# Kernel optimization log

Hardware: AMD Instinct MI355X
Metric: run time of the kernel (lower is better)

Reference implementation:

```python
import jax, jax.numpy as jnp
import numpy as np

ATT = 256  # att_fc_size
MIN_W = 32  # min_width_feat
EPS = 1e-5  # InstanceNorm eps


def setup_inputs() -> dict:
    key = jax.random.key(0)
    ks = jax.random.split(key, 16)
    B, C, H, W = 32, 256, 128, 256
    hid = 256
    s = 0.02
    inp = {
        'features': jax.random.normal(ks[0], (B, C, H, W), jnp.float32),
        'prev_attn_weights': jax.random.uniform(ks[1], (B, H), jnp.float32),
        'coverage_vector': jax.random.uniform(ks[2], (B, H), jnp.float32) * 2.0,
        'hidden_h': jax.random.normal(ks[3], (1, B, hid), jnp.float32),
        # dense_width: Linear(min_width, 1)
        'w_width': jax.random.normal(ks[4], (MIN_W, 1), jnp.float32) * s,
        'b_width': jnp.zeros((1,), jnp.float32),
        # dense_enc: Linear(C, att)
        'w_enc': jax.random.normal(ks[5], (C, ATT), jnp.float32) * s,
        'b_enc': jnp.zeros((ATT,), jnp.float32),
        # conv_block: Conv1d(2, 16, k=15, pad=7)  (OIW layout)
        'conv_w': jax.random.normal(ks[6], (16, 2, 15), jnp.float32) * s,
        'conv_b': jnp.zeros((16,), jnp.float32),
        # dense_conv_block: Linear(16, att)
        'w_cb': jax.random.normal(ks[7], (16, ATT), jnp.float32) * s,
        'b_cb': jnp.zeros((ATT,), jnp.float32),
        # dense_hidden: Linear(hidden, att)
        'w_hid': jax.random.normal(ks[8], (hid, ATT), jnp.float32) * s,
        'b_hid': jnp.zeros((ATT,), jnp.float32),
        # dense_align: Linear(att, 1)
        'w_align': jax.random.normal(ks[9], (ATT, 1), jnp.float32) * s,
        'b_align': jnp.zeros((1,), jnp.float32),
    }
    return inp


def reference(features, prev_attn_weights, coverage_vector, hidden_h,
              w_width, b_width, w_enc, b_enc, conv_w, conv_b,
              w_cb, b_cb, w_hid, b_hid, w_align, b_align):
    B, C, H, W = features.shape
    # AdaptiveMaxPool2d((None, MIN_W)) with W % MIN_W == 0 -> uniform window max
    hf = features.reshape(B, C, H, MIN_W, W // MIN_W).max(axis=-1)  # (B,C,H,MIN_W)
    # dense_width -> (B,C,H)
    h_features = (jnp.einsum('bchm,mo->bcho', hf, w_width) + b_width)[..., 0]
    # branch 1: dense_enc on (B,H,C)
    s = jnp.einsum('bhc,ca->bha', h_features.transpose(0, 2, 1), w_enc) + b_enc
    # location + coverage channels: (B,2,H)
    cat = jnp.stack([prev_attn_weights, jnp.clip(coverage_vector, 0.0, 1.0)], axis=1)
    # InstanceNorm1d (no affine): per (b, channel) over H
    mu = cat.mean(axis=-1, keepdims=True)
    var = cat.var(axis=-1, keepdims=True)
    cat = (cat - mu) * jax.lax.rsqrt(var + EPS)
    # Conv1d(2 -> 16, k=15, pad=7)
    conv = jax.lax.conv_general_dilated(
        cat, conv_w, window_strides=(1,), padding=[(7, 7)],
        dimension_numbers=('NCH', 'OIH', 'NCH')) + conv_b[None, :, None]  # (B,16,H)
    s = s + jnp.einsum('bhk,ka->bha', conv.transpose(0, 2, 1), w_cb) + b_cb
    # hidden branch: (1,B,hid) -> (1,B,att) -> (B,1,att), broadcasts over H
    hsum = (jnp.einsum('lbd,da->lba', hidden_h, w_hid) + b_hid).transpose(1, 0, 2)
    s = s + hsum
    s = jnp.tanh(s)
    align_score = jnp.einsum('bha,ao->bho', s, w_align) + b_align  # (B,H,1)
    attn = jax.nn.softmax(align_score, axis=1)  # softmax over H
    # context: features^T(H<->W) @ attn -> (B,C,W)
    context = jnp.einsum('bchw,bh->bcw', features, attn[..., 0])
    return context, attn[..., 0]
```

## Files before the change

### kernel.cpp

```cpp
#include <hip/hip_runtime.h>
#include <hip/hip_bf16.h>

#define B_DIM 32
#define C_DIM 256
#define H_DIM 128
#define W_DIM 256
#define ATT_DIM 256

__global__ __launch_bounds__(256) void k1_pool_width(
    const float* __restrict__ feat, const float* __restrict__ w_width,
    const float* __restrict__ b_width, float* __restrict__ hfT)
{
  const int lane = threadIdx.x & 63;
  const long r = (long)blockIdx.x * 4 + (threadIdx.x >> 6);
  const float* p = feat + (size_t)r * W_DIM + lane * 4;
  float4 v4 = *reinterpret_cast<const float4*>(p);
  float v = fmaxf(fmaxf(v4.x, v4.y), fmaxf(v4.z, v4.w));
  v = fmaxf(v, __shfl_xor(v, 1));
  float contrib = (lane & 1) ? 0.0f : v * w_width[lane >> 1];
#pragma unroll
  for (int off = 32; off >= 1; off >>= 1) contrib += __shfl_xor(contrib, off);
  if (lane == 0) {
    int b = (int)(r >> 15);
    int c = ((int)r >> 7) & 255;
    int h = (int)r & 127;
    hfT[((size_t)(b * H_DIM + h)) * C_DIM + c] = contrib + b_width[0];
  }
}

__global__ __launch_bounds__(128) void k2_norm_conv(
    const float* __restrict__ prev, const float* __restrict__ cov,
    const float* __restrict__ conv_w, const float* __restrict__ conv_b,
    float* __restrict__ convT)
{
  const int b = blockIdx.x, h = threadIdx.x;
  const int lane = h & 63, wid = h >> 6;
  __shared__ float n0[H_DIM], n1[H_DIM];
  __shared__ float ws4[2][4];
  __shared__ float cw[16 * 2 * 15];
  for (int i = h; i < 480; i += 128) cw[i] = conv_w[i];
  float x0 = prev[b * H_DIM + h];
  float x1 = cov[b * H_DIM + h];
  x1 = fminf(fmaxf(x1, 0.0f), 1.0f);
  float s0 = x0, q0 = x0 * x0, s1 = x1, q1 = x1 * x1;
#pragma unroll
  for (int off = 32; off >= 1; off >>= 1) {
    s0 += __shfl_xor(s0, off); q0 += __shfl_xor(q0, off);
    s1 += __shfl_xor(s1, off); q1 += __shfl_xor(q1, off);
  }
  if (lane == 0) { ws4[wid][0] = s0; ws4[wid][1] = q0; ws4[wid][2] = s1; ws4[wid][3] = q1; }
  __syncthreads();
  float S0 = ws4[0][0] + ws4[1][0], Q0 = ws4[0][1] + ws4[1][1];
  float S1 = ws4[0][2] + ws4[1][2], Q1 = ws4[0][3] + ws4[1][3];
  const float rH = 1.0f / H_DIM;
  float mu0 = S0 * rH, mu1 = S1 * rH;
  float var0 = Q0 * rH - mu0 * mu0;
  float var1 = Q1 * rH - mu1 * mu1;
  float inv0 = 1.0f / sqrtf(var0 + 1e-5f);
  float inv1 = 1.0f / sqrtf(var1 + 1e-5f);
  n0[h] = (x0 - mu0) * inv0;
  n1[h] = (x1 - mu1) * inv1;
  __syncthreads();
  float o[16];
#pragma unroll
  for (int k = 0; k < 16; k++) o[k] = conv_b[k];
#pragma unroll
  for (int j = 0; j < 15; j++) {
    int hh = h - 7 + j;
    if (hh >= 0 && hh < H_DIM) {
      float f0 = n0[hh], f1 = n1[hh];
#pragma unroll
      for (int k = 0; k < 16; k++)
        o[k] += f0 * cw[k * 30 + j] + f1 * cw[k * 30 + 15 + j];
    }
  }
  float* outp = convT + ((size_t)(b * H_DIM + h)) * 16;
#pragma unroll
  for (int k = 0; k < 16; k++) outp[k] = o[k];
}

__global__ __launch_bounds__(256) void k2b_hsum(
    const float* __restrict__ hidden, const float* __restrict__ w_hid,
    const float* __restrict__ b_hid, const float* __restrict__ b_enc,
    const float* __restrict__ b_cb, float* __restrict__ hsum)
{
  const int b = blockIdx.x, a = threadIdx.x;
  float acc = b_hid[a] + b_enc[a] + b_cb[a];
  const float* hb = hidden + b * 256;
#pragma unroll 4
  for (int d = 0; d < 256; d++) acc += hb[d] * w_hid[d * ATT_DIM + a];
  hsum[b * ATT_DIM + a] = acc;
}

__global__ __launch_bounds__(256) void k3_gemm_align(
    const float* __restrict__ hfT, const float* __restrict__ convT,
    const float* __restrict__ hsum, const float* __restrict__ w_enc,
    const float* __restrict__ w_cb, const float* __restrict__ w_align,
    const float* __restrict__ b_align, float* __restrict__ align_out)
{
  __shared__ float At[C_DIM][20];
  __shared__ float Ct[16][17];
  __shared__ float red[16][ATT_DIM];
  const int tid = threadIdx.x;
  const int m0 = blockIdx.x * 16;
  const int b = m0 >> 7;
#pragma unroll
  for (int i = 0; i < 16; i++)
    At[tid][i] = hfT[(size_t)(m0 + i) * C_DIM + tid];
  {
    int m = tid >> 4, k = tid & 15;
    Ct[k][m] = convT[(size_t)m0 * 16 + tid];
  }
  __syncthreads();
  float acc[16];
#pragma unroll
  for (int m = 0; m < 16; m++) acc[m] = 0.0f;
  const float* wep = w_enc + tid;
#pragma unroll 4
  for (int k = 0; k < C_DIM; k++) {
    float bv = wep[k * ATT_DIM];
    const float4 a0 = *reinterpret_cast<const float4*>(&At[k][0]);
    const float4 a1 = *reinterpret_cast<const float4*>(&At[k][4]);
    const float4 a2 = *reinterpret_cast<const float4*>(&At[k][8]);
    const float4 a3 = *reinterpret_cast<const float4*>(&At[k][12]);
    acc[0] += a0.x * bv; acc[1] += a0.y * bv; acc[2] += a0.z * bv; acc[3] += a0.w * bv;
    acc[4] += a1.x * bv; acc[5] += a1.y * bv; acc[6] += a1.z * bv; acc[7] += a1.w * bv;
    acc[8] += a2.x * bv; acc[9] += a2.y * bv; acc[10] += a2.z * bv; acc[11] += a2.w * bv;
    acc[12] += a3.x * bv; acc[13] += a3.y * bv; acc[14] += a3.z * bv; acc[15] += a3.w * bv;
  }
#pragma unroll
  for (int k = 0; k < 16; k++) {
    float bv = w_cb[k * ATT_DIM + tid];
#pragma unroll
    for (int m = 0; m < 16; m++) acc[m] += Ct[k][m] * bv;
  }
  const float hs = hsum[b * ATT_DIM + tid];
  const float wa = w_align[tid];
#pragma unroll
  for (int m = 0; m < 16; m++)
    red[m][tid] = tanhf(acc[m] + hs) * wa;
  __syncthreads();
  const int lane = tid & 63, wid = tid >> 6;
  const float ba = b_align[0];
  for (int m = wid; m < 16; m += 4) {
    float s = red[m][lane] + red[m][lane + 64] + red[m][lane + 128] + red[m][lane + 192];
#pragma unroll
    for (int off = 32; off >= 1; off >>= 1) s += __shfl_xor(s, off);
    if (lane == 0) align_out[m0 + m] = s + ba;
  }
}

__global__ __launch_bounds__(128) void k4_softmax(
    const float* __restrict__ align, float* __restrict__ attn)
{
  const int b = blockIdx.x, h = threadIdx.x;
  const int lane = h & 63, wid = h >> 6;
  __shared__ float sm[2], ss[2];
  float x = align[b * H_DIM + h];
  float m = x;
#pragma unroll
  for (int off = 32; off >= 1; off >>= 1) m = fmaxf(m, __shfl_xor(m, off));
  if (lane == 0) sm[wid] = m;
  __syncthreads();
  m = fmaxf(sm[0], sm[1]);
  float e = expf(x - m);
  float s = e;
#pragma unroll
  for (int off = 32; off >= 1; off >>= 1) s += __shfl_xor(s, off);
  if (lane == 0) ss[wid] = s;
  __syncthreads();
  s = ss[0] + ss[1];
  attn[b * H_DIM + h] = e / s;
}

__global__ __launch_bounds__(256) void k5_context(
    const float* __restrict__ feat, const float* __restrict__ attn,
    float* __restrict__ ctx)
{
  const int bc = blockIdx.x;
  const int b = bc >> 8;
  const int tid = threadIdx.x;
  __shared__ float at[H_DIM];
  if (tid < H_DIM) at[tid] = attn[(b << 7) + tid];
  __syncthreads();
  const int g = tid >> 6, lane = tid & 63;
  const float* base = feat + (size_t)bc * H_DIM * W_DIM;
  float4 acc = make_float4(0.f, 0.f, 0.f, 0.f);
  for (int h = g; h < H_DIM; h += 4) {
    float4 v = *reinterpret_cast<const float4*>(base + h * W_DIM + lane * 4);
    float a = at[h];
    acc.x += v.x * a; acc.y += v.y * a; acc.z += v.z * a; acc.w += v.w * a;
  }
  __shared__ float4 part[4][64];
  part[g][lane] = acc;
  __syncthreads();
  if (tid < 64) {
    float4 r0 = part[0][tid], r1 = part[1][tid], r2 = part[2][tid], r3 = part[3][tid];
    float4 o;
    o.x = r0.x + r1.x + r2.x + r3.x;
    o.y = r0.y + r1.y + r2.y + r3.y;
    o.z = r0.z + r1.z + r2.z + r3.z;
    o.w = r0.w + r1.w + r2.w + r3.w;
    *reinterpret_cast<float4*>(ctx + (size_t)bc * W_DIM + tid * 4) = o;
  }
}

extern "C" void kernel_launch(void* const* d_in, const int* in_sizes, int n_in,
                              void* d_out, int out_size, void* d_ws, size_t ws_size,
                              hipStream_t stream)
{
  const float* feat    = (const float*)d_in[0];
  const float* prev    = (const float*)d_in[1];
  const float* cov     = (const float*)d_in[2];
  const float* hidden  = (const float*)d_in[3];
  const float* w_width = (const float*)d_in[4];
  const float* b_width = (const float*)d_in[5];
  const float* w_enc   = (const float*)d_in[6];
  const float* b_enc   = (const float*)d_in[7];
  const float* conv_w  = (const float*)d_in[8];
  const float* conv_b  = (const float*)d_in[9];
  const float* w_cb    = (const float*)d_in[10];
  const float* b_cb    = (const float*)d_in[11];
  const float* w_hid   = (const float*)d_in[12];
  const float* b_hid   = (const float*)d_in[13];
  const float* w_align = (const float*)d_in[14];
  const float* b_align = (const float*)d_in[15];

  float* ctx_out  = (float*)d_out;
  float* attn_out = (float*)d_out + (size_t)B_DIM * C_DIM * W_DIM;

  float* ws    = (float*)d_ws;
  float* hfT   = ws;
  float* convT = hfT + 1048576;
  float* hsum  = convT + 65536;
  float* align = hsum + 8192;

  k1_pool_width<<<dim3((B_DIM * C_DIM * H_DIM) / 4), dim3(256), 0, stream>>>(
      feat, w_width, b_width, hfT);
  k2_norm_conv<<<dim3(B_DIM), dim3(128), 0, stream>>>(prev, cov, conv_w, conv_b, convT);
  k2b_hsum<<<dim3(B_DIM), dim3(256), 0, stream>>>(hidden, w_hid, b_hid, b_enc, b_cb, hsum);
  k3_gemm_align<<<dim3((B_DIM * H_DIM) / 16), dim3(256), 0, stream>>>(
      hfT, convT, hsum, w_enc, w_cb, w_align, b_align, align);
  k4_softmax<<<dim3(B_DIM), dim3(128), 0, stream>>>(align, attn_out);
  k5_context<<<dim3(B_DIM * C_DIM), dim3(256), 0, stream>>>(feat, attn_out, ctx_out);
}
```

Baseline: 493.5 us.

## Fuse small kernels, reverse context block order for L2 reuse, shrink GEMM tile

Merges the pooling, norm+conv and hidden-projection kernels into one launch. The pooling part now gives each block one (b,c) slab and writes hf in B,C,H layout with coalesced stores. The softmax moves into the context kernel, which runs its blocks in reverse order so recently pooled feature slabs may still sit in L2. The align GEMM tile shrinks from 16 to 8 rows to launch more blocks. This cuts launch count and the scattered transposed stores, at the cost of recomputing the softmax in every context block.

Result: faster. 400.6 us (-18.8%).

```diff
diff --git a/kernel.cpp b/kernel.cpp
--- a/kernel.cpp
+++ b/kernel.cpp
@@ -7,142 +7,150 @@
 #define W_DIM 256
 #define ATT_DIM 256
 
-__global__ __launch_bounds__(256) void k1_pool_width(
+__global__ __launch_bounds__(256) void ka_fused(
     const float* __restrict__ feat, const float* __restrict__ w_width,
-    const float* __restrict__ b_width, float* __restrict__ hfT)
-{
-  const int lane = threadIdx.x & 63;
-  const long r = (long)blockIdx.x * 4 + (threadIdx.x >> 6);
-  const float* p = feat + (size_t)r * W_DIM + lane * 4;
-  float4 v4 = *reinterpret_cast<const float4*>(p);
-  float v = fmaxf(fmaxf(v4.x, v4.y), fmaxf(v4.z, v4.w));
-  v = fmaxf(v, __shfl_xor(v, 1));
-  float contrib = (lane & 1) ? 0.0f : v * w_width[lane >> 1];
-#pragma unroll
-  for (int off = 32; off >= 1; off >>= 1) contrib += __shfl_xor(contrib, off);
-  if (lane == 0) {
-    int b = (int)(r >> 15);
-    int c = ((int)r >> 7) & 255;
-    int h = (int)r & 127;
-    hfT[((size_t)(b * H_DIM + h)) * C_DIM + c] = contrib + b_width[0];
-  }
-}
-
-__global__ __launch_bounds__(128) void k2_norm_conv(
+    const float* __restrict__ b_width,
     const float* __restrict__ prev, const float* __restrict__ cov,
     const float* __restrict__ conv_w, const float* __restrict__ conv_b,
-    float* __restrict__ convT)
-{
-  const int b = blockIdx.x, h = threadIdx.x;
-  const int lane = h & 63, wid = h >> 6;
-  __shared__ float n0[H_DIM], n1[H_DIM];
-  __shared__ float ws4[2][4];
-  __shared__ float cw[16 * 2 * 15];
-  for (int i = h; i < 480; i += 128) cw[i] = conv_w[i];
-  float x0 = prev[b * H_DIM + h];
-  float x1 = cov[b * H_DIM + h];
-  x1 = fminf(fmaxf(x1, 0.0f), 1.0f);
-  float s0 = x0, q0 = x0 * x0, s1 = x1, q1 = x1 * x1;
-#pragma unroll
-  for (int off = 32; off >= 1; off >>= 1) {
-    s0 += __shfl_xor(s0, off); q0 += __shfl_xor(q0, off);
-    s1 += __shfl_xor(s1, off); q1 += __shfl_xor(q1, off);
-  }
-  if (lane == 0) { ws4[wid][0] = s0; ws4[wid][1] = q0; ws4[wid][2] = s1; ws4[wid][3] = q1; }
-  __syncthreads();
-  float S0 = ws4[0][0] + ws4[1][0], Q0 = ws4[0][1] + ws4[1][1];
-  float S1 = ws4[0][2] + ws4[1][2], Q1 = ws4[0][3] + ws4[1][3];
-  const float rH = 1.0f / H_DIM;
-  float mu0 = S0 * rH, mu1 = S1 * rH;
-  float var0 = Q0 * rH - mu0 * mu0;
-  float var1 = Q1 * rH - mu1 * mu1;
-  float inv0 = 1.0f / sqrtf(var0 + 1e-5f);
-  float inv1 = 1.0f / sqrtf(var1 + 1e-5f);
-  n0[h] = (x0 - mu0) * inv0;
-  n1[h] = (x1 - mu1) * inv1;
-  __syncthreads();
-  float o[16];
-#pragma unroll
-  for (int k = 0; k < 16; k++) o[k] = conv_b[k];
-#pragma unroll
-  for (int j = 0; j < 15; j++) {
-    int hh = h - 7 + j;
-    if (hh >= 0 && hh < H_DIM) {
-      float f0 = n0[hh], f1 = n1[hh];
-#pragma unroll
-      for (int k = 0; k < 16; k++)
-        o[k] += f0 * cw[k * 30 + j] + f1 * cw[k * 30 + 15 + j];
-    }
-  }
-  float* outp = convT + ((size_t)(b * H_DIM + h)) * 16;
-#pragma unroll
-  for (int k = 0; k < 16; k++) outp[k] = o[k];
-}
-
-__global__ __launch_bounds__(256) void k2b_hsum(
     const float* __restrict__ hidden, const float* __restrict__ w_hid,
     const float* __restrict__ b_hid, const float* __restrict__ b_enc,
-    const float* __restrict__ b_cb, float* __restrict__ hsum)
-{
-  const int b = blockIdx.x, a = threadIdx.x;
-  float acc = b_hid[a] + b_enc[a] + b_cb[a];
-  const float* hb = hidden + b * 256;
-#pragma unroll 4
-  for (int d = 0; d < 256; d++) acc += hb[d] * w_hid[d * ATT_DIM + a];
-  hsum[b * ATT_DIM + a] = acc;
-}
-
-__global__ __launch_bounds__(256) void k3_gemm_align(
-    const float* __restrict__ hfT, const float* __restrict__ convT,
+    const float* __restrict__ b_cb,
+    float* __restrict__ hf, float* __restrict__ convT, float* __restrict__ hsum)
+{
+  const int tid = threadIdx.x;
+  const int bid = blockIdx.x;
+
+  if (bid < 8192) {
+    __shared__ float res[H_DIM];
+    const int lane = tid & 63, wid = tid >> 6;
+    const float wv = w_width[lane >> 1] * 0.5f;
+    const float bw = b_width[0];
+    const float* base = feat + (size_t)bid * H_DIM * W_DIM + lane * 4;
+#pragma unroll 4
+    for (int i = 0; i < 32; i++) {
+      const int h = wid + 4 * i;
+      float4 v4 = *reinterpret_cast<const float4*>(base + (size_t)h * W_DIM);
+      float v = fmaxf(fmaxf(v4.x, v4.y), fmaxf(v4.z, v4.w));
+      v = fmaxf(v, __shfl_xor(v, 1));
+      float contrib = v * wv;
+#pragma unroll
+      for (int off = 32; off >= 1; off >>= 1) contrib += __shfl_xor(contrib, off);
+      if (lane == 0) res[h] = contrib + bw;
+    }
+    __syncthreads();
+    if (tid < H_DIM)
+      hf[(size_t)bid * H_DIM + tid] = res[tid];
+  } else if (bid < 8224) {
+    const int b = bid - 8192;
+    __shared__ float n0[H_DIM], n1[H_DIM];
+    __shared__ float ws4[2][4];
+    __shared__ float cw[480];
+    for (int i = tid; i < 480; i += 256) cw[i] = conv_w[i];
+    const int lane = tid & 63, wv2 = tid >> 6;
+    float x0 = 0.f, x1 = 0.f;
+    if (tid < 128) {
+      x0 = prev[b * H_DIM + tid];
+      x1 = cov[b * H_DIM + tid];
+      x1 = fminf(fmaxf(x1, 0.0f), 1.0f);
+      float s0 = x0, q0 = x0 * x0, s1 = x1, q1 = x1 * x1;
+#pragma unroll
+      for (int off = 32; off >= 1; off >>= 1) {
+        s0 += __shfl_xor(s0, off); q0 += __shfl_xor(q0, off);
+        s1 += __shfl_xor(s1, off); q1 += __shfl_xor(q1, off);
+      }
+      if (lane == 0) { ws4[wv2][0] = s0; ws4[wv2][1] = q0; ws4[wv2][2] = s1; ws4[wv2][3] = q1; }
+    }
+    __syncthreads();
+    if (tid < 128) {
+      float S0 = ws4[0][0] + ws4[1][0], Q0 = ws4[0][1] + ws4[1][1];
+      float S1 = ws4[0][2] + ws4[1][2], Q1 = ws4[0][3] + ws4[1][3];
+      const float rH = 1.0f / H_DIM;
+      float mu0 = S0 * rH, mu1 = S1 * rH;
+      float inv0 = 1.0f / sqrtf(Q0 * rH - mu0 * mu0 + 1e-5f);
+      float inv1 = 1.0f / sqrtf(Q1 * rH - mu1 * mu1 + 1e-5f);
+      n0[tid] = (x0 - mu0) * inv0;
+      n1[tid] = (x1 - mu1) * inv1;
+    }
+    __syncthreads();
+    if (tid < 128) {
+      float o[16];
+#pragma unroll
+      for (int k = 0; k < 16; k++) o[k] = conv_b[k];
+#pragma unroll
+      for (int j = 0; j < 15; j++) {
+        int hh = tid - 7 + j;
+        if (hh >= 0 && hh < H_DIM) {
+          float f0 = n0[hh], f1 = n1[hh];
+#pragma unroll
+          for (int k = 0; k < 16; k++)
+            o[k] += f0 * cw[k * 30 + j] + f1 * cw[k * 30 + 15 + j];
+        }
+      }
+      float* outp = convT + ((size_t)(b * H_DIM + tid)) * 16;
+#pragma unroll
+      for (int k = 0; k < 16; k++) outp[k] = o[k];
+    }
+  } else {
+    const int b = bid - 8224;
+    const int a = tid;
+    float acc = b_hid[a] + b_enc[a] + b_cb[a];
+    const float* hb = hidden + b * 256;
+#pragma unroll 4
+    for (int d = 0; d < 256; d++) acc += hb[d] * w_hid[d * ATT_DIM + a];
+    hsum[b * ATT_DIM + a] = acc;
+  }
+}
+
+__global__ __launch_bounds__(256) void kb_gemm_align(
+    const float* __restrict__ hf, const float* __restrict__ convT,
     const float* __restrict__ hsum, const float* __restrict__ w_enc,
     const float* __restrict__ w_cb, const float* __restrict__ w_align,
     const float* __restrict__ b_align, float* __restrict__ align_out)
 {
-  __shared__ float At[C_DIM][20];
-  __shared__ float Ct[16][17];
-  __shared__ float red[16][ATT_DIM];
+  __shared__ float At[C_DIM][12];
+  __shared__ float Ct[16][9];
+  __shared__ float red[8][ATT_DIM];
   const int tid = threadIdx.x;
-  const int m0 = blockIdx.x * 16;
+  const int m0 = blockIdx.x * 8;
   const int b = m0 >> 7;
-#pragma unroll
-  for (int i = 0; i < 16; i++)
-    At[tid][i] = hfT[(size_t)(m0 + i) * C_DIM + tid];
-  {
+  const int h0 = m0 & 127;
+  const float* hp = hf + ((size_t)(b * C_DIM + tid)) * H_DIM + h0;
+  float4 r0 = *reinterpret_cast<const float4*>(hp);
+  float4 r1 = *reinterpret_cast<const float4*>(hp + 4);
+  *reinterpret_cast<float4*>(&At[tid][0]) = r0;
+  *reinterpret_cast<float4*>(&At[tid][4]) = r1;
+  if (tid < 128) {
     int m = tid >> 4, k = tid & 15;
-    Ct[k][m] = convT[(size_t)m0 * 16 + tid];
-  }
-  __syncthreads();
-  float acc[16];
-#pragma unroll
-  for (int m = 0; m < 16; m++) acc[m] = 0.0f;
+    Ct[k][m] = convT[(size_t)(b * H_DIM + h0) * 16 + tid];
+  }
+  __syncthreads();
+  float acc[8];
+#pragma unroll
+  for (int m = 0; m < 8; m++) acc[m] = 0.0f;
   const float* wep = w_enc + tid;
 #pragma unroll 4
   for (int k = 0; k < C_DIM; k++) {
     float bv = wep[k * ATT_DIM];
     const float4 a0 = *reinterpret_cast<const float4*>(&At[k][0]);
     const float4 a1 = *reinterpret_cast<const float4*>(&At[k][4]);
-    const float4 a2 = *reinterpret_cast<const float4*>(&At[k][8]);
-    const float4 a3 = *reinterpret_cast<const float4*>(&At[k][12]);
     acc[0] += a0.x * bv; acc[1] += a0.y * bv; acc[2] += a0.z * bv; acc[3] += a0.w * bv;
     acc[4] += a1.x * bv; acc[5] += a1.y * bv; acc[6] += a1.z * bv; acc[7] += a1.w * bv;
-    acc[8] += a2.x * bv; acc[9] += a2.y * bv; acc[10] += a2.z * bv; acc[11] += a2.w * bv;
-    acc[12] += a3.x * bv; acc[13] += a3.y * bv; acc[14] += a3.z * bv; acc[15] += a3.w * bv;
   }
 #pragma unroll
   for (int k = 0; k < 16; k++) {
     float bv = w_cb[k * ATT_DIM + tid];
 #pragma unroll
-    for (int m = 0; m < 16; m++) acc[m] += Ct[k][m] * bv;
+    for (int m = 0; m < 8; m++) acc[m] += Ct[k][m] * bv;
   }
   const float hs = hsum[b * ATT_DIM + tid];
   const float wa = w_align[tid];
 #pragma unroll
-  for (int m = 0; m < 16; m++)
+  for (int m = 0; m < 8; m++)
     red[m][tid] = tanhf(acc[m] + hs) * wa;
   __syncthreads();
   const int lane = tid & 63, wid = tid >> 6;
   const float ba = b_align[0];
-  for (int m = wid; m < 16; m += 4) {
+  for (int m = wid; m < 8; m += 4) {
     float s = red[m][lane] + red[m][lane + 64] + red[m][lane + 128] + red[m][lane + 192];
 #pragma unroll
     for (int off = 32; off >= 1; off >>= 1) s += __shfl_xor(s, off);
@@ -150,44 +158,37 @@
   }
 }
 
-__global__ __launch_bounds__(128) void k4_softmax(
-    const float* __restrict__ align, float* __restrict__ attn)
-{
-  const int b = blockIdx.x, h = threadIdx.x;
-  const int lane = h & 63, wid = h >> 6;
-  __shared__ float sm[2], ss[2];
-  float x = align[b * H_DIM + h];
-  float m = x;
-#pragma unroll
-  for (int off = 32; off >= 1; off >>= 1) m = fmaxf(m, __shfl_xor(m, off));
-  if (lane == 0) sm[wid] = m;
-  __syncthreads();
-  m = fmaxf(sm[0], sm[1]);
-  float e = expf(x - m);
-  float s = e;
-#pragma unroll
-  for (int off = 32; off >= 1; off >>= 1) s += __shfl_xor(s, off);
-  if (lane == 0) ss[wid] = s;
-  __syncthreads();
-  s = ss[0] + ss[1];
-  attn[b * H_DIM + h] = e / s;
-}
-
-__global__ __launch_bounds__(256) void k5_context(
-    const float* __restrict__ feat, const float* __restrict__ attn,
-    float* __restrict__ ctx)
-{
-  const int bc = blockIdx.x;
-  const int b = bc >> 8;
+__global__ __launch_bounds__(256) void kc_context(
+    const float* __restrict__ feat, const float* __restrict__ align,
+    float* __restrict__ attn_out, float* __restrict__ ctx)
+{
+  const int bc = 8191 - blockIdx.x;
+  const int b = bc >> 8, c = bc & 255;
   const int tid = threadIdx.x;
-  __shared__ float at[H_DIM];
-  if (tid < H_DIM) at[tid] = attn[(b << 7) + tid];
-  __syncthreads();
+  __shared__ float al[H_DIM], at[H_DIM];
+  if (tid < H_DIM) al[tid] = align[(b << 7) + tid];
+  __syncthreads();
+  if (tid < 64) {
+    float a0 = al[tid], a1 = al[tid + 64];
+    float mx = fmaxf(a0, a1);
+#pragma unroll
+    for (int off = 32; off >= 1; off >>= 1) mx = fmaxf(mx, __shfl_xor(mx, off));
+    float e0 = expf(a0 - mx), e1 = expf(a1 - mx);
+    float s = e0 + e1;
+#pragma unroll
+    for (int off = 32; off >= 1; off >>= 1) s += __shfl_xor(s, off);
+    float inv = 1.0f / s;
+    at[tid] = e0 * inv;
+    at[tid + 64] = e1 * inv;
+  }
+  __syncthreads();
+  if (c == 0 && tid < H_DIM) attn_out[(b << 7) + tid] = at[tid];
   const int g = tid >> 6, lane = tid & 63;
-  const float* base = feat + (size_t)bc * H_DIM * W_DIM;
+  const float* base = feat + (size_t)bc * H_DIM * W_DIM + lane * 4;
   float4 acc = make_float4(0.f, 0.f, 0.f, 0.f);
+#pragma unroll 4
   for (int h = g; h < H_DIM; h += 4) {
-    float4 v = *reinterpret_cast<const float4*>(base + h * W_DIM + lane * 4);
+    float4 v = *reinterpret_cast<const float4*>(base + (size_t)h * W_DIM);
     float a = at[h];
     acc.x += v.x * a; acc.y += v.y * a; acc.z += v.z * a; acc.w += v.w * a;
   }
@@ -230,17 +231,16 @@
   float* attn_out = (float*)d_out + (size_t)B_DIM * C_DIM * W_DIM;
 
   float* ws    = (float*)d_ws;
-  float* hfT   = ws;
-  float* convT = hfT + 1048576;
+  float* hf    = ws;
+  float* convT = hf + 1048576;
   float* hsum  = convT + 65536;
   float* align = hsum + 8192;
 
-  k1_pool_width<<<dim3((B_DIM * C_DIM * H_DIM) / 4), dim3(256), 0, stream>>>(
-      feat, w_width, b_width, hfT);
-  k2_norm_conv<<<dim3(B_DIM), dim3(128), 0, stream>>>(prev, cov, conv_w, conv_b, convT);
-  k2b_hsum<<<dim3(B_DIM), dim3(256), 0, stream>>>(hidden, w_hid, b_hid, b_enc, b_cb, hsum);
-  k3_gemm_align<<<dim3((B_DIM * H_DIM) / 16), dim3(256), 0, stream>>>(
-      hfT, convT, hsum, w_enc, w_cb, w_align, b_align, align);
-  k4_softmax<<<dim3(B_DIM), dim3(128), 0, stream>>>(align, attn_out);
-  k5_context<<<dim3(B_DIM * C_DIM), dim3(256), 0, stream>>>(feat, attn_out, ctx_out);
-}
+  ka_fused<<<dim3(8192 + 32 + 32), dim3(256), 0, stream>>>(
+      feat, w_width, b_width, prev, cov, conv_w, conv_b,
+      hidden, w_hid, b_hid, b_enc, b_cb, hf, convT, hsum);
+  kb_gemm_align<<<dim3((B_DIM * H_DIM) / 8), dim3(256), 0, stream>>>(
+      hf, convT, hsum, w_enc, w_cb, w_align, b_align, align);
+  kc_context<<<dim3(B_DIM * C_DIM), dim3(256), 0, stream>>>(
+      feat, align, attn_out, ctx_out);
+}
```
